# Kernel optimization log

Hardware: AMD Instinct MI355X
Metric: run time of the kernel (lower is better)

## Reference

```python
import jax, jax.numpy as jnp
import numpy as np

E = 256  # embedding_dim

def setup_inputs() -> dict:
    key = jax.random.key(0)
    k1, k2, k3 = jax.random.split(key, 3)
    B, P, N, D = 32, 4, 1024, E
    x = jax.random.normal(k1, (B, P, N, D), dtype=jnp.float32)
    W_qkv = jax.random.normal(k2, (D, 1 + 2 * E), dtype=jnp.float32) * (1.0 / np.sqrt(D))
    b_qkv = jnp.zeros((1 + 2 * E,), dtype=jnp.float32)
    W_o = jax.random.normal(k3, (E, E), dtype=jnp.float32) * (1.0 / np.sqrt(E))
    b_o = jnp.zeros((E,), dtype=jnp.float32)
    return {"x": x, "W_qkv": W_qkv, "b_qkv": b_qkv, "W_o": W_o, "b_o": b_o}

def reference(x, W_qkv, b_qkv, W_o, b_o):
    # qkv projection: [B,P,N,D] @ [D,1+2E] -> [B,P,N,1+2E]
    qkv = jnp.einsum('bpnd,de->bpne', x, W_qkv) + b_qkv
    q = qkv[..., :1]                 # [B,P,N,1]
    k = qkv[..., 1:1 + E]            # [B,P,N,E]
    v = jax.nn.relu(qkv[..., 1 + E:])  # [B,P,N,E]
    # softmax over patch axis N (axis=2)
    context_scores = jax.nn.softmax(q, axis=2)
    # context vector: sum over N of k * scores -> [B,P,1,E]
    context_vector = jnp.sum(k * context_scores, axis=2, keepdims=True)
    # broadcast-multiply with relu(v): [B,P,N,E] * [B,P,1,E]
    updated_values = v * context_vector
    # output projection
    out = jnp.einsum('bpnd,de->bpne', updated_values, W_o) + b_o
    return out
```

## Files before the change

### kernel.cpp

```cpp
#include <hip/hip_runtime.h>
#include <hip/hip_bf16.h>

typedef float f32x4 __attribute__((ext_vector_type(4)));
typedef short s16x8 __attribute__((ext_vector_type(8)));
typedef __bf16 bf16x8 __attribute__((ext_vector_type(8)));
typedef unsigned short u16;

#define NSEQ 1024
#define EDIM 256

__device__ __forceinline__ u16 f2bf(float f){
  union { float f; unsigned u; } v; v.f = f;
  unsigned r = v.u + 0x7FFF + ((v.u >> 16) & 1);
  return (u16)(r >> 16);
}
__device__ __forceinline__ float bf2f(u16 b){
  union { float f; unsigned u; } v; v.u = ((unsigned)b) << 16;
  return v.f;
}

template <typename V>
__device__ __forceinline__ auto mfma_impl(V a, V b, f32x4 c, int)
    -> decltype(__builtin_amdgcn_mfma_f32_16x16x32_bf16(a, b, c, 0, 0, 0)) {
  return __builtin_amdgcn_mfma_f32_16x16x32_bf16(a, b, c, 0, 0, 0);
}
template <typename V>
__device__ __forceinline__ f32x4 mfma_impl(V a, V b, f32x4 c, long){
  bf16x8 ab = __builtin_bit_cast(bf16x8, a);
  bf16x8 bb = __builtin_bit_cast(bf16x8, b);
  return __builtin_amdgcn_mfma_f32_16x16x32_bf16(ab, bb, c, 0, 0, 0);
}
__device__ __forceinline__ f32x4 mfma16(s16x8 a, s16x8 b, f32x4 c){
  return mfma_impl(a, b, c, 0);
}

__device__ __forceinline__ void gload_lds16(const u16* g, u16* l){
  __builtin_amdgcn_global_load_lds((const __attribute__((address_space(1))) void*)g,
                                   (__attribute__((address_space(3))) void*)l, 16, 0, 0);
}

__global__ void k0_prep(const float* __restrict__ Wqkv, const float* __restrict__ Wo,
                        u16* __restrict__ wvf, u16* __restrict__ wof, float* __restrict__ wqc){
  int t = blockIdx.x * 256 + threadIdx.x;
  if (t < 16384){
    int which = t >> 13;
    int slot  = t & 8191;
    int l  = slot & 63;
    int nt = (slot >> 6) & 1;
    int ks = (slot >> 7) & 7;
    int c  = (slot >> 10) & 7;
    int row = ks*32 + 8*(l>>4);
    int col = c*32 + nt*16 + (l&15);
    s16x8 o8;
    if (which == 0){
      for (int j=0;j<8;j++) o8[j] = (short)f2bf(Wqkv[(size_t)(row+j)*513 + 257 + col]);
      *(s16x8*)(wvf + (size_t)slot*8) = o8;
    } else {
      for (int j=0;j<8;j++) o8[j] = (short)f2bf(Wo[(size_t)(row+j)*256 + col]);
      *(s16x8*)(wof + (size_t)slot*8) = o8;
    }
  } else if (t < 16384 + 256){
    int d = t - 16384;
    wqc[d] = Wqkv[(size_t)d*513];
  }
}

__global__ void k1_qfrag(const float* __restrict__ x, const float* __restrict__ wqc,
                         const float* __restrict__ bqkv, u16* __restrict__ xf, float* __restrict__ q){
  int bp = blockIdx.x >> 6, rt = blockIdx.x & 63;
  const float* xt = x + ((size_t)bp*NSEQ + rt*16) * EDIM;
  __shared__ float xl[16][260];
  int tid = threadIdx.x;
  for (int i=0;i<4;i++){
    int idx = tid + i*256;
    float4 vv = ((const float4*)xt)[idx];
    int row = idx >> 6, c4 = idx & 63;
    *(float4*)&xl[row][c4*4] = vv;
  }
  __syncthreads();
  int l = tid & 63, w = tid >> 6;
  int lo = l & 15, hi = l >> 4;
  for (int kk=0;kk<2;kk++){
    int ks = w*2 + kk;
    int k0 = ks*32 + 8*hi;
    s16x8 o8;
    for (int j=0;j<8;j++) o8[j] = (short)f2bf(xl[lo][k0+j]);
    size_t fo = ((((size_t)bp*64 + rt)*8 + ks)*64 + l) * 8;
    *(s16x8*)(xf + fo) = o8;
  }
  int c = l*4;
  float4 wv4 = *(const float4*)(wqc + c);
  float b0 = bqkv[0];
  for (int r=0;r<4;r++){
    int row = w*4 + r;
    float4 xv = *(float4*)&xl[row][c];
    float p = xv.x*wv4.x + xv.y*wv4.y + xv.z*wv4.z + xv.w*wv4.w;
    for (int o=32;o;o>>=1) p += __shfl_down(p, o);
    if (l == 0) q[(size_t)bp*NSEQ + rt*16 + row] = p + b0;
  }
}

__global__ void k2_softmax(const float* __restrict__ q, float* __restrict__ s){
  int bp = blockIdx.x, tid = threadIdx.x;
  float4 v = ((const float4*)(q + (size_t)bp*NSEQ))[tid];
  __shared__ float red[8];
  float m = fmaxf(fmaxf(v.x, v.y), fmaxf(v.z, v.w));
  for (int o=32;o;o>>=1) m = fmaxf(m, __shfl_xor(m, o));
  if ((tid & 63) == 0) red[tid >> 6] = m;
  __syncthreads();
  m = fmaxf(fmaxf(red[0], red[1]), fmaxf(red[2], red[3]));
  float e0 = expf(v.x - m), e1 = expf(v.y - m), e2 = expf(v.z - m), e3 = expf(v.w - m);
  float sum = e0 + e1 + e2 + e3;
  for (int o=32;o;o>>=1) sum += __shfl_xor(sum, o);
  if ((tid & 63) == 0) red[4 + (tid >> 6)] = sum;
  __syncthreads();
  float inv = 1.0f / (red[4] + red[5] + red[6] + red[7]);
  float4 o4 = {e0*inv, e1*inv, e2*inv, e3*inv};
  ((float4*)(s + (size_t)bp*NSEQ))[tid] = o4;
}

__global__ void k3_tpart(const u16* __restrict__ xf, const float* __restrict__ s, float* __restrict__ tp){
  int bp = blockIdx.x >> 3, ks = blockIdx.x & 7;
  int tid = threadIdx.x, l = tid & 63, w = tid >> 6;
  int lo = l & 15, hi = l >> 4;
  const float* sb = s + (size_t)bp*NSEQ;
  float acc[8];
  for (int j=0;j<8;j++) acc[j] = 0.f;
  for (int rti=0; rti<16; rti++){
    int rt = w*16 + rti;
    s16x8 v = *(const s16x8*)(xf + ((((size_t)bp*64 + rt)*8 + ks)*64 + l)*8);
    float sv = sb[rt*16 + lo];
    for (int j=0;j<8;j++) acc[j] += sv * bf2f((u16)v[j]);
  }
  for (int j=0;j<8;j++)
    for (int m=1;m<16;m<<=1) acc[j] += __shfl_xor(acc[j], m);
  __shared__ float red[4][32];
  if (lo == 0)
    for (int j=0;j<8;j++) red[w][8*hi + j] = acc[j];
  __syncthreads();
  if (tid < 32){
    float t = red[0][tid] + red[1][tid] + red[2][tid] + red[3][tid];
    tp[(size_t)bp*EDIM + ks*32 + tid] = t;
  }
}

__global__ void k4_cv(const float* __restrict__ tp, const float* __restrict__ Wqkv,
                      const float* __restrict__ bqkv, float* __restrict__ cv){
  int bp = blockIdx.x, e = threadIdx.x;
  __shared__ float tl[256];
  tl[e] = tp[(size_t)bp*EDIM + e];
  __syncthreads();
  float acc = bqkv[1 + e];
  for (int d=0;d<256;d++) acc += tl[d] * Wqkv[(size_t)d*513 + 1 + e];
  cv[(size_t)bp*EDIM + e] = acc;
}

__global__ __launch_bounds__(256) void k5_main(
    const u16* __restrict__ xf, const u16* __restrict__ wvf, const u16* __restrict__ wof,
    const float* __restrict__ bqkv, const float* __restrict__ bo,
    const float* __restrict__ cv, float* __restrict__ out){
  int bp = blockIdx.x >> 4, rt = blockIdx.x & 15;
  int tid = threadIdx.x, l = tid & 63, w = tid >> 6;
  int lo = l & 15, hi = l >> 4;
  __shared__ u16 WBUF[2][16][512];
  __shared__ u16 HB[4][16][40];

  s16x8 af[8];
  {
    const u16* src = xf + ((((size_t)bp*64 + rt*4 + w)*8)*64 + l)*8;
#pragma unroll
    for (int ks=0;ks<8;ks++) af[ks] = *(const s16x8*)(src + (size_t)ks*512);
  }
  const float* cvb = cv + (size_t)bp*EDIM;

  {
    const u16* gsrc = wvf + (size_t)(w*4)*512 + l*8;
#pragma unroll
    for (int i=0;i<4;i++) gload_lds16(gsrc + i*512, &WBUF[0][w*4 + i][0]);
  }
  __syncthreads();

  s16x8 hf[8];

#pragma unroll
  for (int c=0;c<8;c++){
    int cur = c & 1;
    {
      const u16* nsrc = (c < 7) ? (wvf + (size_t)(c+1)*8192) : wof;
      const u16* gsrc = nsrc + (size_t)(w*4)*512 + l*8;
#pragma unroll
      for (int i=0;i<4;i++) gload_lds16(gsrc + i*512, &WBUF[cur^1][w*4 + i][0]);
    }
#pragma unroll
    for (int nt=0;nt<2;nt++){
      f32x4 acc = {0.f,0.f,0.f,0.f};
#pragma unroll
      for (int ks=0;ks<8;ks++){
        s16x8 b = *(const s16x8*)&WBUF[cur][ks*2 + nt][l*8];
        acc = mfma16(af[ks], b, acc);
      }
      int col = c*32 + nt*16 + lo;
      float bv = bqkv[257 + col], cs = cvb[col];
#pragma unroll
      for (int r=0;r<4;r++){
        float h = acc[r] + bv;
        h = h > 0.f ? h : 0.f;
        HB[w][hi*4 + r][nt*16 + lo] = f2bf(h * cs);
      }
    }
    hf[c] = *(const s16x8*)&HB[w][lo][8*hi];
    __syncthreads();
  }

  float* ob = out + ((size_t)bp*NSEQ + rt*64 + w*16) * EDIM;
#pragma unroll
  for (int c2=0;c2<8;c2++){
    int cur = c2 & 1;
    if (c2 < 7){
      const u16* gsrc = wof + (size_t)(c2+1)*8192 + (size_t)(w*4)*512 + l*8;
#pragma unroll
      for (int i=0;i<4;i++) gload_lds16(gsrc + i*512, &WBUF[cur^1][w*4 + i][0]);
    }
#pragma unroll
    for (int nt=0;nt<2;nt++){
      f32x4 acc = {0.f,0.f,0.f,0.f};
#pragma unroll
      for (int ks=0;ks<8;ks++){
        s16x8 b = *(const s16x8*)&WBUF[cur][ks*2 + nt][l*8];
        acc = mfma16(hf[ks], b, acc);
      }
      int col = c2*32 + nt*16 + lo;
      float bb = bo[col];
#pragma unroll
      for (int r=0;r<4;r++)
        ob[(size_t)(hi*4 + r)*EDIM + col] = acc[r] + bb;
    }
    if (c2 < 7) __syncthreads();
  }
}

extern "C" void kernel_launch(void* const* d_in, const int* in_sizes, int n_in,
                              void* d_out, int out_size, void* d_ws, size_t ws_size,
                              hipStream_t stream){
  const float* x    = (const float*)d_in[0];
  const float* Wqkv = (const float*)d_in[1];
  const float* bqkv = (const float*)d_in[2];
  const float* Wo   = (const float*)d_in[3];
  const float* bo   = (const float*)d_in[4];
  float* out = (float*)d_out;
  char* ws = (char*)d_ws;
  u16*   xf  = (u16*)(ws);
  u16*   wvf = (u16*)(ws + 67108864);
  u16*   wof = (u16*)(ws + 67239936);
  float* q   = (float*)(ws + 67371008);
  float* s   = (float*)(ws + 67895296);
  float* tp  = (float*)(ws + 68419584);
  float* cvv = (float*)(ws + 69468160);
  float* wqc = (float*)(ws + 69599232);

  hipLaunchKernelGGL(k0_prep,    dim3(65),   dim3(256), 0, stream, Wqkv, Wo, wvf, wof, wqc);
  hipLaunchKernelGGL(k1_qfrag,   dim3(8192), dim3(256), 0, stream, x, wqc, bqkv, xf, q);
  hipLaunchKernelGGL(k2_softmax, dim3(128),  dim3(256), 0, stream, q, s);
  hipLaunchKernelGGL(k3_tpart,   dim3(1024), dim3(256), 0, stream, xf, s, tp);
  hipLaunchKernelGGL(k4_cv,      dim3(128),  dim3(256), 0, stream, tp, Wqkv, bqkv, cvv);
  hipLaunchKernelGGL(k5_main,    dim3(2048), dim3(256), 0, stream, xf, wvf, wof, bqkv, bo, cvv, out);
}
```

Measured before the change: 131.9 us.

## Process two row tiles per wave with triple-buffered weight staging in k5_main

Each wave now computes two 16-row tiles, so every weight fragment read from LDS feeds two MFMAs, and the grid is halved to 1024 blocks. The two GEMM phases are merged into one 16-chunk loop with a triple-buffered LDS ring, prefetched two chunks ahead. Full __syncthreads calls are replaced by explicit vmcnt waits plus raw barriers. This raises register and LDS pressure (launch bounds set to 2 blocks) and the hand-counted vmcnt values are fragile.

```diff
diff --git a/kernel.cpp b/kernel.cpp
--- a/kernel.cpp
+++ b/kernel.cpp
@@ -8,6 +8,8 @@
 
 #define NSEQ 1024
 #define EDIM 256
+
+#define WAITVM(N) asm volatile("s_waitcnt vmcnt(" #N ")" ::: "memory")
 
 __device__ __forceinline__ u16 f2bf(float f){
   union { float f; unsigned u; } v; v.f = f;
@@ -155,87 +157,99 @@
   cv[(size_t)bp*EDIM + e] = acc;
 }
 
-__global__ __launch_bounds__(256) void k5_main(
+__global__ __launch_bounds__(256, 2) void k5_main(
     const u16* __restrict__ xf, const u16* __restrict__ wvf, const u16* __restrict__ wof,
     const float* __restrict__ bqkv, const float* __restrict__ bo,
     const float* __restrict__ cv, float* __restrict__ out){
-  int bp = blockIdx.x >> 4, rt = blockIdx.x & 15;
+  int bp = blockIdx.x >> 3, rt = blockIdx.x & 7;
   int tid = threadIdx.x, l = tid & 63, w = tid >> 6;
   int lo = l & 15, hi = l >> 4;
-  __shared__ u16 WBUF[2][16][512];
-  __shared__ u16 HB[4][16][40];
-
-  s16x8 af[8];
+  __shared__ u16 WBUF[3][16][512];
+  __shared__ u16 HB[4][2][16][40];
+
+  s16x8 af0[8], af1[8];
   {
-    const u16* src = xf + ((((size_t)bp*64 + rt*4 + w)*8)*64 + l)*8;
-#pragma unroll
-    for (int ks=0;ks<8;ks++) af[ks] = *(const s16x8*)(src + (size_t)ks*512);
+    const u16* src0 = xf + ((((size_t)bp*64 + rt*8 + 2*w + 0)*8)*64 + l)*8;
+    const u16* src1 = src0 + 4096;
+#pragma unroll
+    for (int ks=0;ks<8;ks++){
+      af0[ks] = *(const s16x8*)(src0 + (size_t)ks*512);
+      af1[ks] = *(const s16x8*)(src1 + (size_t)ks*512);
+    }
   }
   const float* cvb = cv + (size_t)bp*EDIM;
-
-  {
-    const u16* gsrc = wvf + (size_t)(w*4)*512 + l*8;
-#pragma unroll
-    for (int i=0;i<4;i++) gload_lds16(gsrc + i*512, &WBUF[0][w*4 + i][0]);
-  }
-  __syncthreads();
-
-  s16x8 hf[8];
-
-#pragma unroll
-  for (int c=0;c<8;c++){
-    int cur = c & 1;
-    {
-      const u16* nsrc = (c < 7) ? (wvf + (size_t)(c+1)*8192) : wof;
-      const u16* gsrc = nsrc + (size_t)(w*4)*512 + l*8;
-#pragma unroll
-      for (int i=0;i<4;i++) gload_lds16(gsrc + i*512, &WBUF[cur^1][w*4 + i][0]);
-    }
-#pragma unroll
-    for (int nt=0;nt<2;nt++){
-      f32x4 acc = {0.f,0.f,0.f,0.f};
+  float* ob0 = out + ((size_t)bp*NSEQ + (rt*8 + 2*w + 0)*16) * EDIM;
+  float* ob1 = ob0 + 16*EDIM;
+
+  auto stage = [&](int chunk, int buf){
+    const u16* base = (chunk < 8) ? (wvf + (size_t)chunk*8192) : (wof + (size_t)(chunk-8)*8192);
+    const u16* gsrc = base + (size_t)(w*4)*512 + l*8;
+#pragma unroll
+    for (int i=0;i<4;i++) gload_lds16(gsrc + i*512, &WBUF[buf][w*4 + i][0]);
+  };
+
+  stage(0, 0);
+  stage(1, 1);
+  WAITVM(4);
+  __builtin_amdgcn_s_barrier();
+  __builtin_amdgcn_sched_barrier(0);
+
+  s16x8 hf0[8], hf1[8];
+
+#pragma unroll
+  for (int c=0;c<16;c++){
+    const int buf = c % 3;
+    f32x4 acc00 = {0.f,0.f,0.f,0.f}, acc01 = acc00, acc10 = acc00, acc11 = acc00;
+    auto do_mfma = [&](const s16x8 (&A0)[8], const s16x8 (&A1)[8]){
 #pragma unroll
       for (int ks=0;ks<8;ks++){
-        s16x8 b = *(const s16x8*)&WBUF[cur][ks*2 + nt][l*8];
-        acc = mfma16(af[ks], b, acc);
+        s16x8 b0 = *(const s16x8*)&WBUF[buf][ks*2 + 0][l*8];
+        s16x8 b1 = *(const s16x8*)&WBUF[buf][ks*2 + 1][l*8];
+        acc00 = mfma16(A0[ks], b0, acc00);
+        acc10 = mfma16(A1[ks], b0, acc10);
+        acc01 = mfma16(A0[ks], b1, acc01);
+        acc11 = mfma16(A1[ks], b1, acc11);
       }
-      int col = c*32 + nt*16 + lo;
-      float bv = bqkv[257 + col], cs = cvb[col];
+    };
+    if (c < 8) do_mfma(af0, af1); else do_mfma(hf0, hf1);
+
+    if (c < 8){
+      int colA = c*32 + lo, colB = colA + 16;
+      float bvA = bqkv[257 + colA], bvB = bqkv[257 + colB];
+      float csA = cvb[colA],        csB = cvb[colB];
 #pragma unroll
       for (int r=0;r<4;r++){
-        float h = acc[r] + bv;
-        h = h > 0.f ? h : 0.f;
-        HB[w][hi*4 + r][nt*16 + lo] = f2bf(h * cs);
+        float h00 = acc00[r] + bvA, h01 = acc01[r] + bvB;
+        float h10 = acc10[r] + bvA, h11 = acc11[r] + bvB;
+        HB[w][0][hi*4 + r][lo]      = f2bf(h00 > 0.f ? h00*csA : 0.f);
+        HB[w][0][hi*4 + r][16 + lo] = f2bf(h01 > 0.f ? h01*csB : 0.f);
+        HB[w][1][hi*4 + r][lo]      = f2bf(h10 > 0.f ? h10*csA : 0.f);
+        HB[w][1][hi*4 + r][16 + lo] = f2bf(h11 > 0.f ? h11*csB : 0.f);
       }
-    }
-    hf[c] = *(const s16x8*)&HB[w][lo][8*hi];
-    __syncthreads();
-  }
-
-  float* ob = out + ((size_t)bp*NSEQ + rt*64 + w*16) * EDIM;
-#pragma unroll
-  for (int c2=0;c2<8;c2++){
-    int cur = c2 & 1;
-    if (c2 < 7){
-      const u16* gsrc = wof + (size_t)(c2+1)*8192 + (size_t)(w*4)*512 + l*8;
-#pragma unroll
-      for (int i=0;i<4;i++) gload_lds16(gsrc + i*512, &WBUF[cur^1][w*4 + i][0]);
-    }
-#pragma unroll
-    for (int nt=0;nt<2;nt++){
-      f32x4 acc = {0.f,0.f,0.f,0.f};
-#pragma unroll
-      for (int ks=0;ks<8;ks++){
-        s16x8 b = *(const s16x8*)&WBUF[cur][ks*2 + nt][l*8];
-        acc = mfma16(hf[ks], b, acc);
+      hf0[c] = *(const s16x8*)&HB[w][0][lo][8*hi];
+      hf1[c] = *(const s16x8*)&HB[w][1][lo][8*hi];
+    } else {
+      int c2 = c - 8;
+      int colA = c2*32 + lo, colB = colA + 16;
+      float bbA = bo[colA], bbB = bo[colB];
+#pragma unroll
+      for (int r=0;r<4;r++){
+        ob0[(size_t)(hi*4 + r)*EDIM + colA] = acc00[r] + bbA;
+        ob0[(size_t)(hi*4 + r)*EDIM + colB] = acc01[r] + bbB;
+        ob1[(size_t)(hi*4 + r)*EDIM + colA] = acc10[r] + bbA;
+        ob1[(size_t)(hi*4 + r)*EDIM + colB] = acc11[r] + bbB;
       }
-      int col = c2*32 + nt*16 + lo;
-      float bb = bo[col];
-#pragma unroll
-      for (int r=0;r<4;r++)
-        ob[(size_t)(hi*4 + r)*EDIM + col] = acc[r] + bb;
-    }
-    if (c2 < 7) __syncthreads();
+    }
+
+    if (c + 2 <= 15) stage(c + 2, (c + 2) % 3);
+
+    if (c < 8)       WAITVM(4);
+    else if (c < 14) WAITVM(20);
+    else if (c == 14) WAITVM(16);
+    if (c < 15){
+      __builtin_amdgcn_s_barrier();
+      __builtin_amdgcn_sched_barrier(0);
+    }
   }
 }
 
@@ -263,5 +277,5 @@
   hipLaunchKernelGGL(k2_softmax, dim3(128),  dim3(256), 0, stream, q, s);
   hipLaunchKernelGGL(k3_tpart,   dim3(1024), dim3(256), 0, stream, xf, s, tp);
   hipLaunchKernelGGL(k4_cv,      dim3(128),  dim3(256), 0, stream, tp, Wqkv, bqkv, cvv);
-  hipLaunchKernelGGL(k5_main,    dim3(2048), dim3(256), 0, stream, xf, wvf, wof, bqkv, bo, cvv, out);
-}
+  hipLaunchKernelGGL(k5_main,    dim3(1024), dim3(256), 0, stream, xf, wvf, wof, bqkv, bo, cvv, out);
+}
```

Result: no change. 130.1 us (-1.3%).
